# Kernel optimization log

Measured on AMD Instinct MI355X. Metric: run time of the kernel, lower is better.

The kernel has to match this reference:

```python
import jax, jax.numpy as jnp
import numpy as np

DIM = 256
N_STATE = 8
DT_RANK = 16  # ceil(dim/16)
D_CONV = 4
HIDDEN = 128  # dim * rank_ratio
EPS = 1e-6


def rmsnorm(x, w):
    # matches torch: x / (||x||_2 / sqrt(d) + eps) * w
    norm = jnp.sqrt(jnp.sum(x * x, axis=-1, keepdims=True))
    return x / (norm / np.sqrt(x.shape[-1]) + EPS) * w


def dwconv1d(x, w, b, pad_l, pad_r):
    # x: (b, l, c); w: (c, 1, k) depthwise
    out = jax.lax.conv_general_dilated(
        x.transpose(0, 2, 1), w, window_strides=(1,),
        padding=[(pad_l, pad_r)], dimension_numbers=('NCH', 'OIH', 'NCH'),
        feature_group_count=w.shape[0])
    return (out + b[None, :, None]).transpose(0, 2, 1)


def selective_scan(x, delta, A, Bm, Cm, D):
    # x, delta: (b,l,d); A: (d,n); Bm, Cm: (b,l,n); D: (d,)
    dA = jnp.exp(delta[..., None] * A)                     # (b,l,d,n)
    dBx = (delta * x)[..., None] * Bm[:, :, None, :]       # (b,l,d,n)

    def step(h, inp):
        dA_t, dBx_t, C_t = inp
        h = dA_t * h + dBx_t                               # (b,d,n)
        y = jnp.einsum('bdn,bn->bd', h, C_t)
        return h, y

    h0 = jnp.zeros((x.shape[0],) + A.shape, dtype=x.dtype)
    _, ys = jax.lax.scan(step, h0,
                         (dA.transpose(1, 0, 2, 3), dBx.transpose(1, 0, 2, 3),
                          Cm.transpose(1, 0, 2)))
    return ys.transpose(1, 0, 2) + x * D                   # (b,l,d)


def mamba_branch(x, ctx, conv_w, conv_b, xproj_w, dtproj_w, dtproj_b, A_log, D):
    xc = jax.nn.silu(dwconv1d(x, conv_w, conv_b, D_CONV - 1, 0))  # causal conv
    x_dbl = ctx @ xproj_w.T                                  # (b,l,r+2n)
    dt, Bm, Cm = jnp.split(x_dbl, [DT_RANK, DT_RANK + N_STATE], axis=-1)
    delta = jax.nn.softplus(dt @ dtproj_w.T + dtproj_b)
    A = -jnp.exp(A_log)
    return selective_scan(xc, delta, A, Bm, Cm, D)


def setup_inputs() -> dict:
    key = jax.random.key(0)
    ks = jax.random.split(key, 24)
    B, L, D = 4, 64 * 64, DIM
    s = 0.02
    A_log_init = jnp.log(jnp.broadcast_to(jnp.arange(1, N_STATE + 1, dtype=jnp.float32), (D, N_STATE)))
    dt_bias = jnp.full((D,), jnp.log(jnp.expm1(0.01)), dtype=jnp.float32)
    inp = {
        'x0': jax.random.normal(ks[0], (B, L, D), jnp.float32),
        'x1': jax.random.normal(ks[1], (B, L, D), jnp.float32),
        'w_norm0': jnp.ones((D,), jnp.float32),
        'w_norm1': jnp.ones((D,), jnp.float32),
        'in_proj_w': jax.random.normal(ks[2], (2 * D, D), jnp.float32) * s,
        'conv_w_f': jax.random.normal(ks[3], (D, 1, D_CONV), jnp.float32) * 0.3,
        'conv_b_f': jnp.zeros((D,), jnp.float32),
        'xproj_w_f': jax.random.normal(ks[4], (DT_RANK + 2 * N_STATE, D), jnp.float32) * s,
        'dtproj_w_f': jax.random.normal(ks[5], (D, DT_RANK), jnp.float32) * 0.1,
        'dtproj_b_f': dt_bias,
        'A_log_f': A_log_init,
        'D_f': jnp.ones((D,), jnp.float32),
        'conv_w_bw': jax.random.normal(ks[6], (D, 1, D_CONV), jnp.float32) * 0.3,
        'conv_b_bw': jnp.zeros((D,), jnp.float32),
        'xproj_w_bw': jax.random.normal(ks[7], (DT_RANK + 2 * N_STATE, D), jnp.float32) * s,
        'dtproj_w_bw': jax.random.normal(ks[8], (D, DT_RANK), jnp.float32) * 0.1,
        'dtproj_b_bw': dt_bias,
        'A_log_bw': A_log_init,
        'D_bw': jnp.ones((D,), jnp.float32),
        'norm_y_w': jnp.ones((D,), jnp.float32),
        'out_proj_w': jax.random.normal(ks[9], (D, D), jnp.float32) * s,
        'fc1_w': jax.random.normal(ks[10], (HIDDEN, D), jnp.float32) * s,
        'dw_w': jax.random.normal(ks[11], (HIDDEN, 1, 3), jnp.float32) * 0.3,
        'dw_b': jnp.zeros((HIDDEN,), jnp.float32),
        'fc2_w': jax.random.normal(ks[12], (D, HIDDEN), jnp.float32) * s,
    }
    return inp


def reference(x0, x1, w_norm0, w_norm1, in_proj_w, conv_w_f, conv_b_f, xproj_w_f,
              dtproj_w_f, dtproj_b_f, A_log_f, D_f, conv_w_bw, conv_b_bw,
              xproj_w_bw, dtproj_w_bw, dtproj_b_bw, A_log_bw, D_bw, norm_y_w,
              out_proj_w, fc1_w, dw_w, dw_b, fc2_w):
    residual = x0
    h0 = rmsnorm(x0, w_norm0)
    h1 = rmsnorm(x1, w_norm1)
    # cross-Mamba: main stream x0 -> x,z; extra_emb x1 -> dt/B/C
    xz = h0 @ in_proj_w.T
    xin, z = jnp.split(xz, 2, axis=-1)
    y_f = mamba_branch(xin, h1, conv_w_f, conv_b_f, xproj_w_f, dtproj_w_f,
                       dtproj_b_f, A_log_f, D_f)
    y_b = jnp.flip(mamba_branch(jnp.flip(xin, 1), jnp.flip(h1, 1), conv_w_bw,
                                conv_b_bw, xproj_w_bw, dtproj_w_bw, dtproj_b_bw,
                                A_log_bw, D_bw), 1)
    y = (y_f + y_b) * 0.5          # if_devide_out=True (bidirectional)
    y = rmsnorm(y, norm_y_w)       # use_norm=True
    y = y * jax.nn.silu(z)
    x = y @ out_proj_w.T + residual
    # LowRankFeedForward (dropout = identity at eval)
    m = x @ fc1_w.T
    m = jax.nn.silu(dwconv1d(m, dw_w, dw_b, 1, 1))
    m = m @ fc2_w.T
    return x + m
```

## Files before the change

kernel.cpp:

```cpp
#include <hip/hip_runtime.h>
#include <math.h>
#include <cstddef>

#define BB 4
#define LL 4096
#define DD 256
#define NST 8
#define RANK 16
#define HID 128
#define BL (BB*LL)
#define BLD ((size_t)BL*DD)
#define CH 256
#define CLEN 16
#define XZS 512

typedef __bf16 bf16x8 __attribute__((ext_vector_type(8)));
typedef float  f32x4  __attribute__((ext_vector_type(4)));

__device__ __forceinline__ float siluf(float x){ return x / (1.f + __expf(-x)); }
__device__ __forceinline__ float softplus_fast(float x){
  float r = __logf(1.f + __expf(x));
  return x > 15.f ? x : r;
}
__device__ __forceinline__ unsigned short f2bf(float x){
  union { float f; unsigned u; } v; v.f = x;
  unsigned r = v.u + 0x7fffu + ((v.u >> 16) & 1u);
  return (unsigned short)(r >> 16);
}
__device__ __forceinline__ float bf2f(unsigned short u){
  union { unsigned u32; float f; } c; c.u32 = ((unsigned)u) << 16;
  return c.f;
}

__global__ __launch_bounds__(64) void rms_kernel(
    const float* __restrict__ x0, const float* __restrict__ w0, unsigned short* __restrict__ o0b,
    const float* __restrict__ x1, const float* __restrict__ w1, unsigned short* __restrict__ o1b)
{
  const float* x; const float* w; unsigned short* o;
  if (blockIdx.y == 0){ x = x0; w = w0; o = o0b; } else { x = x1; w = w1; o = o1b; }
  size_t tok = blockIdx.x;
  int lane = threadIdx.x;
  float4 v = ((const float4*)(x + tok*DD))[lane];
  float s = v.x*v.x + v.y*v.y + v.z*v.z + v.w*v.w;
  #pragma unroll
  for (int m = 1; m < 64; m <<= 1) s += __shfl_xor(s, m, 64);
  float scale = 1.f / (sqrtf(s) * (1.f/16.f) + 1e-6f);
  float4 wv = ((const float4*)w)[lane];
  ushort4 r;
  r.x = f2bf(v.x*scale*wv.x); r.y = f2bf(v.y*scale*wv.y);
  r.z = f2bf(v.z*scale*wv.z); r.w = f2bf(v.w*scale*wv.w);
  ((ushort4*)(o + tok*DD))[lane] = r;
}

__global__ __launch_bounds__(256) void cvt1_kernel(
    const float* __restrict__ s, unsigned short* __restrict__ d, int n)
{
  int i = blockIdx.x*256 + threadIdx.x;
  if (i < n) d[i] = f2bf(s[i]);
}
__global__ __launch_bounds__(256) void cvt5_kernel(
    const float* __restrict__ s0, const float* __restrict__ s1,
    const float* __restrict__ s2, const float* __restrict__ s3,
    const float* __restrict__ s4, unsigned short* __restrict__ d)
{
  int i = blockIdx.x*256 + threadIdx.x;
  if (i >= 147456) return;
  float v;
  if (i < 8192)        v = s0[i];
  else if (i < 16384)  v = s1[i - 8192];
  else if (i < 81920)  v = s2[i - 16384];
  else if (i < 114688) v = s3[i - 81920];
  else                 v = s4[i - 114688];
  d[i] = f2bf(v);
}

template<int EPI>
__global__ __launch_bounds__(256) void gemm_mfma(
    const unsigned short* __restrict__ A, const unsigned short* __restrict__ Bw,
    float* __restrict__ C, const float* __restrict__ Add,
    unsigned short* __restrict__ Cb, int M, int ldc, int K)
{
  constexpr int BK = 32, PAD = 8;
  __shared__ __align__(16) unsigned short As[64][BK+PAD];
  __shared__ __align__(16) unsigned short Bs[64][BK+PAD];
  int tid  = threadIdx.x;
  int row0 = blockIdx.x * 64;
  int col0 = blockIdx.y * 64;
  int wave = tid >> 6, lane = tid & 63;
  int wm = (wave >> 1) * 32, wn = (wave & 1) * 32;
  int lm = lane & 15, kq = lane >> 4;
  int sr = tid >> 2, sc8 = (tid & 3) * 8;

  f32x4 acc[2][2];
  #pragma unroll
  for (int i = 0; i < 2; i++)
    #pragma unroll
    for (int j = 0; j < 2; j++) acc[i][j] = (f32x4){0.f,0.f,0.f,0.f};

  for (int k0 = 0; k0 < K; k0 += BK){
    *(int4*)&As[sr][sc8] = *(const int4*)&A [(size_t)(row0 + sr)*K + k0 + sc8];
    *(int4*)&Bs[sr][sc8] = *(const int4*)&Bw[(size_t)(col0 + sr)*K + k0 + sc8];
    __syncthreads();
    bf16x8 af[2], bfv[2];
    #pragma unroll
    for (int i = 0; i < 2; i++) af[i]  = *(const bf16x8*)&As[wm + i*16 + lm][kq*8];
    #pragma unroll
    for (int j = 0; j < 2; j++) bfv[j] = *(const bf16x8*)&Bs[wn + j*16 + lm][kq*8];
    #pragma unroll
    for (int i = 0; i < 2; i++)
      #pragma unroll
      for (int j = 0; j < 2; j++)
        acc[i][j] = __builtin_amdgcn_mfma_f32_16x16x32_bf16(af[i], bfv[j], acc[i][j], 0, 0, 0);
    __syncthreads();
  }

  #pragma unroll
  for (int i = 0; i < 2; i++){
    int rbase = row0 + wm + i*16 + kq*4;
    #pragma unroll
    for (int j = 0; j < 2; j++){
      int col = col0 + wn + j*16 + lm;
      #pragma unroll
      for (int r = 0; r < 4; r++){
        size_t idx = (size_t)(rbase + r)*ldc + col;
        float v = acc[i][j][r];
        if constexpr (EPI == 1 || EPI == 2) v += Add[idx];
        if constexpr (EPI != 3) C[idx] = v;
        if constexpr (EPI == 1 || EPI == 3) Cb[idx] = f2bf(v);
      }
    }
  }
}

__global__ __launch_bounds__(256) void front_kernel(
    const unsigned short* __restrict__ xz,
    const float* __restrict__ xd,
    const float* __restrict__ cwf, const float* __restrict__ cbf,
    const float* __restrict__ cwb, const float* __restrict__ cbb,
    const float* __restrict__ dtwf, const float* __restrict__ dtbf,
    const float* __restrict__ dtwb, const float* __restrict__ dtbb,
    const float* __restrict__ Alogf, const float* __restrict__ Alogb,
    const float* __restrict__ Dfp, const float* __restrict__ Dbp,
    unsigned int* __restrict__ xde,
    float* __restrict__ Sp, float* __restrict__ Hout)
{
  int chunk = blockIdx.x, b = blockIdx.y, dir = blockIdx.z;
  int s0 = chunk*CLEN;
  int d  = threadIdx.x;

  __shared__ float sdt[CLEN][16];
  __shared__ float sB [CLEN][8];
  __shared__ float sC [CLEN][8];
  #pragma unroll
  for (int e = threadIdx.x; e < CLEN*32; e += 256){
    int lt = e >> 5, col = e & 31;
    int pos = s0 + lt;
    int row = dir ? (LL-1-pos) : pos;
    float v = xd[((size_t)b*LL + row)*64 + dir*32 + col];
    if (col < 16)      sdt[lt][col]    = v;
    else if (col < 24) sB [lt][col-16] = v;
    else               sC [lt][col-24] = v;
  }
  __syncthreads();

  float4 cw = ((const float4*)(dir ? cwb : cwf))[d];
  float cb  = (dir ? cbb : cbf)[d];
  const float* dtw = (dir ? dtwb : dtwf) + d*RANK;
  float4 w0 = ((const float4*)dtw)[0], w1 = ((const float4*)dtw)[1];
  float4 w2 = ((const float4*)dtw)[2], w3 = ((const float4*)dtw)[3];
  float dtb = (dir ? dtbb : dtbf)[d];
  float Dd  = (dir ? Dbp : Dfp)[d];

  const unsigned short* xp = xz + (size_t)b*LL*XZS + d;
  #define LDX(pos) ((pos) >= 0 ? bf2f(xp[(size_t)(dir ? (LL-1-(pos)) : (pos))*XZS]) : 0.f)

  float xv[CLEN+3];
  xv[0] = LDX(s0-3); xv[1] = LDX(s0-2); xv[2] = LDX(s0-1);
  #pragma unroll
  for (int i = 0; i < CLEN; i++) xv[3+i] = LDX(s0+i);
  #undef LDX

  unsigned packX[CLEN];
  #pragma unroll
  for (int i = 0; i < CLEN; i++){
    float xc = cb;
    xc = fmaf(cw.x, xv[i],   xc); xc = fmaf(cw.y, xv[i+1], xc);
    xc = fmaf(cw.z, xv[i+2], xc); xc = fmaf(cw.w, xv[i+3], xc);
    xc = siluf(xc);
    const float* dt = &sdt[i][0];
    float de = dtb;
    de = fmaf(dt[0],w0.x, fmaf(dt[1],w0.y, fmaf(dt[2],w0.z, fmaf(dt[3],w0.w, de))));
    de = fmaf(dt[4],w1.x, fmaf(dt[5],w1.y, fmaf(dt[6],w1.z, fmaf(dt[7],w1.w, de))));
    de = fmaf(dt[8],w2.x, fmaf(dt[9],w2.y, fmaf(dt[10],w2.z, fmaf(dt[11],w2.w, de))));
    de = fmaf(dt[12],w3.x, fmaf(dt[13],w3.y, fmaf(dt[14],w3.z, fmaf(dt[15],w3.w, de))));
    de = softplus_fast(de);
    packX[i] = (unsigned)f2bf(xc) | ((unsigned)f2bf(de) << 16);
  }

  const float* Alog = dir ? Alogb : Alogf;
  float A[NST];
  bool fast = true;
  #pragma unroll
  for (int n = 0; n < NST; n++){
    A[n] = -__expf(Alog[d*NST + n]);
    fast = fast && (fabsf(A[n] + (float)(n+1)) < 1e-3f);
  }
  float h[NST];
  #pragma unroll
  for (int n = 0; n < NST; n++) h[n] = 0.f;
  float S = 0.f;

  unsigned int* xout = xde + ((size_t)(dir*BB + b)*LL + s0)*DD + d;

  if (fast){
    #pragma unroll
    for (int t = 0; t < CLEN; t++){
      unsigned pk = packX[t];
      float xc = bf2f((unsigned short)(pk & 0xffffu));
      float de = bf2f((unsigned short)(pk >> 16));
      S += de;
      float dux = de * xc;
      const float* Bv = &sB[t][0];
      const float* Cv = &sC[t][0];
      float e1 = __expf(-de);
      float dA = e1;
      float acc = xc * Dd;
      h[0] = fmaf(dA, h[0], dux*Bv[0]); acc = fmaf(h[0], Cv[0], acc); dA *= e1;
      h[1] = fmaf(dA, h[1], dux*Bv[1]); acc = fmaf(h[1], Cv[1], acc); dA *= e1;
      h[2] = fmaf(dA, h[2], dux*Bv[2]); acc = fmaf(h[2], Cv[2], acc); dA *= e1;
      h[3] = fmaf(dA, h[3], dux*Bv[3]); acc = fmaf(h[3], Cv[3], acc); dA *= e1;
      h[4] = fmaf(dA, h[4], dux*Bv[4]); acc = fmaf(h[4], Cv[4], acc); dA *= e1;
      h[5] = fmaf(dA, h[5], dux*Bv[5]); acc = fmaf(h[5], Cv[5], acc); dA *= e1;
      h[6] = fmaf(dA, h[6], dux*Bv[6]); acc = fmaf(h[6], Cv[6], acc); dA *= e1;
      h[7] = fmaf(dA, h[7], dux*Bv[7]); acc = fmaf(h[7], Cv[7], acc);
      xout[(size_t)t*DD] = (pk & 0xffff0000u) | (unsigned)f2bf(acc);
    }
  } else {
    #pragma unroll
    for (int t = 0; t < CLEN; t++){
      unsigned pk = packX[t];
      float xc = bf2f((unsigned short)(pk & 0xffffu));
      float de = bf2f((unsigned short)(pk >> 16));
      S += de;
      float dux = de * xc;
      const float* Bv = &sB[t][0];
      const float* Cv = &sC[t][0];
      float acc = xc * Dd;
      #pragma unroll
      for (int n = 0; n < NST; n++){
        h[n] = fmaf(__expf(de*A[n]), h[n], dux*Bv[n]);
        acc = fmaf(h[n], Cv[n], acc);
      }
      xout[(size_t)t*DD] = (pk & 0xffff0000u) | (unsigned)f2bf(acc);
    }
  }

  size_t ob = ((((size_t)dir*CH + chunk)*BB + b)*DD + d)*NST;
  float4 h0v, h1v;
  h0v.x=h[0]; h0v.y=h[1]; h0v.z=h[2]; h0v.w=h[3];
  h1v.x=h[4]; h1v.y=h[5]; h1v.z=h[6]; h1v.w=h[7];
  *(float4*)&Hout[ob]   = h0v; *(float4*)&Hout[ob+4] = h1v;
  Sp[((size_t)(dir*CH + chunk)*BB + b)*DD + d] = S;
}

__global__ __launch_bounds__(64) void scan_p2(
    const float* __restrict__ Sp, float* H,
    const float* __restrict__ Alogf, const float* __restrict__ Alogb)
{
  const int SEGC = CH/8;
  int blk = blockIdx.x;
  int d   = blk & (DD-1);
  int b   = (blk >> 8) & (BB-1);
  int dir = blk >> 10;
  int t   = threadIdx.x;
  int seg = t >> 3, n = t & 7;
  float A = -__expf((dir ? Alogb : Alogf)[d*NST + n]);

  const size_t sstr = (size_t)BB*DD;
  const size_t hstr = (size_t)BB*DD*NST;
  size_t sb = (size_t)dir*CH*sstr + (size_t)b*DD + d;
  size_t hb = (size_t)dir*CH*hstr + ((size_t)b*DD + d)*NST + n;
  int c0 = seg*SEGC;

  float pv[SEGC], hv[SEGC];
  #pragma unroll
  for (int k = 0; k < SEGC; k++){
    pv[k] = Sp[sb + (size_t)(c0+k)*sstr];
    hv[k] = H [hb + (size_t)(c0+k)*hstr];
  }
  float h = 0.f, Ss = 0.f;
  #pragma unroll
  for (int k = 0; k < SEGC; k++){
    Ss += pv[k];
    pv[k] = __expf(pv[k]*A);
    h = fmaf(pv[k], h, hv[k]);
  }
  float pi = __expf(Ss*A), hi = h;
  #pragma unroll
  for (int off = 8; off < 64; off <<= 1){
    float hprev = __shfl_up(hi, off, 64);
    float pprev = __shfl_up(pi, off, 64);
    if (t >= off){ hi = fmaf(pi, hprev, hi); pi *= pprev; }
  }
  float hin = __shfl_up(hi, 8, 64);
  h = (seg == 0) ? 0.f : hin;
  #pragma unroll
  for (int k = 0; k < SEGC; k++){
    size_t idx = hb + (size_t)(c0+k)*hstr;
    H[idx] = h;
    h = fmaf(pv[k], h, hv[k]);
  }
}

__global__ __launch_bounds__(256) void scan_corr(
    const unsigned int* __restrict__ xde,
    const float* __restrict__ xd,
    const float* __restrict__ Alogf, const float* __restrict__ Alogb,
    const float* __restrict__ Hin,
    unsigned short* __restrict__ yf, unsigned short* __restrict__ yb)
{
  int chunk = blockIdx.x, b = blockIdx.y, dir = blockIdx.z;
  int d = threadIdx.x;
  int base = chunk*CLEN;

  __shared__ float sC[CLEN][8];
  if (threadIdx.x < CLEN*8){
    int lt = threadIdx.x >> 3, col = threadIdx.x & 7;
    int pos = base + lt;
    int row = dir ? (LL-1-pos) : pos;
    sC[lt][col] = xd[((size_t)b*LL + row)*64 + dir*32 + 24 + col];
  }
  __syncthreads();

  const float* Alog = dir ? Alogb : Alogf;
  float A[NST];
  bool fast = true;
  #pragma unroll
  for (int n = 0; n < NST; n++){
    A[n] = -__expf(Alog[d*NST + n]);
    fast = fast && (fabsf(A[n] + (float)(n+1)) < 1e-3f);
  }
  float hn[NST];
  {
    size_t ib = ((((size_t)dir*CH + chunk)*BB + b)*DD + d)*NST;
    float4 a0 = *(const float4*)&Hin[ib];
    float4 a1 = *(const float4*)&Hin[ib+4];
    hn[0]=a0.x; hn[1]=a0.y; hn[2]=a0.z; hn[3]=a0.w;
    hn[4]=a1.x; hn[5]=a1.y; hn[6]=a1.z; hn[7]=a1.w;
  }

  const unsigned int* xdep = xde + ((size_t)(dir*BB + b)*LL + base)*DD + d;
  unsigned short* yp = (dir ? yb : yf) + ((size_t)b*LL + base)*DD + d;

  unsigned int pk[CLEN];
  #pragma unroll
  for (int t = 0; t < CLEN; t++) pk[t] = xdep[(size_t)t*DD];

  float S = 0.f;
  if (fast){
    #pragma unroll
    for (int t = 0; t < CLEN; t++){
      float y0 = bf2f((unsigned short)(pk[t] & 0xffffu));
      float de = bf2f((unsigned short)(pk[t] >> 16));
      S += de;
      float E = __expf(-S);
      float q = E;
      float corr = q * (hn[0]*sC[t][0]);
      q *= E; corr = fmaf(q, hn[1]*sC[t][1], corr);
      q *= E; corr = fmaf(q, hn[2]*sC[t][2], corr);
      q *= E; corr = fmaf(q, hn[3]*sC[t][3], corr);
      q *= E; corr = fmaf(q, hn[4]*sC[t][4], corr);
      q *= E; corr = fmaf(q, hn[5]*sC[t][5], corr);
      q *= E; corr = fmaf(q, hn[6]*sC[t][6], corr);
      q *= E; corr = fmaf(q, hn[7]*sC[t][7], corr);
      yp[(size_t)t*DD] = f2bf(y0 + corr);
    }
  } else {
    #pragma unroll
    for (int t = 0; t < CLEN; t++){
      float y0 = bf2f((unsigned short)(pk[t] & 0xffffu));
      float de = bf2f((unsigned short)(pk[t] >> 16));
      S += de;
      float corr = 0.f;
      #pragma unroll
      for (int n = 0; n < NST; n++)
        corr = fmaf(__expf(S*A[n]), hn[n]*sC[t][n], corr);
      yp[(size_t)t*DD] = f2bf(y0 + corr);
    }
  }
}

__global__ __launch_bounds__(64) void combine_kernel(
    const unsigned short* __restrict__ yf, const unsigned short* __restrict__ yb,
    const unsigned short* __restrict__ xz, const float* __restrict__ wn,
    unsigned short* __restrict__ outb)
{
  size_t tok = blockIdx.x;
  int b = (int)(tok / LL), t = (int)(tok % LL);
  int lane = threadIdx.x;
  ushort4 au = ((const ushort4*)(yf + tok*DD))[lane];
  ushort4 cu = ((const ushort4*)(yb + ((size_t)b*LL + (LL-1-t))*DD))[lane];
  float4 v;
  v.x=(bf2f(au.x)+bf2f(cu.x))*0.5f; v.y=(bf2f(au.y)+bf2f(cu.y))*0.5f;
  v.z=(bf2f(au.z)+bf2f(cu.z))*0.5f; v.w=(bf2f(au.w)+bf2f(cu.w))*0.5f;
  float s = v.x*v.x + v.y*v.y + v.z*v.z + v.w*v.w;
  #pragma unroll
  for (int m = 1; m < 64; m <<= 1) s += __shfl_xor(s, m, 64);
  float scale = 1.f / (sqrtf(s)*(1.f/16.f) + 1e-6f);
  float4 wv = ((const float4*)wn)[lane];
  ushort4 zv = *(const ushort4*)&xz[tok*XZS + 256 + lane*4];
  ushort4 r;
  r.x = f2bf(v.x*scale*wv.x*siluf(bf2f(zv.x)));
  r.y = f2bf(v.y*scale*wv.y*siluf(bf2f(zv.y)));
  r.z = f2bf(v.z*scale*wv.z*siluf(bf2f(zv.z)));
  r.w = f2bf(v.w*scale*wv.w*siluf(bf2f(zv.w)));
  ((ushort4*)(outb + tok*DD))[lane] = r;
}

__global__ __launch_bounds__(256) void dwconv3_kernel(
    const float* __restrict__ m, const float* __restrict__ w,
    const float* __restrict__ bi, unsigned short* __restrict__ o)
{
  size_t gid = (size_t)blockIdx.x*256 + threadIdx.x;
  int c = (int)(gid % HID);
  int tok = (int)(gid / HID);
  int b = tok / LL, t = tok % LL;
  float acc = bi[c];
  #pragma unroll
  for (int k = 0; k < 3; k++){
    int tt = t - 1 + k;
    if (tt >= 0 && tt < LL)
      acc = fmaf(w[c*3 + k], m[((size_t)b*LL + tt)*HID + c], acc);
  }
  o[gid] = f2bf(siluf(acc));
}

extern "C" void kernel_launch(void* const* d_in, const int* in_sizes, int n_in,
                              void* d_out, int out_size, void* d_ws, size_t ws_size,
                              hipStream_t stream)
{
  const float* x0        = (const float*)d_in[0];
  const float* x1        = (const float*)d_in[1];
  const float* w_norm0   = (const float*)d_in[2];
  const float* w_norm1   = (const float*)d_in[3];
  const float* in_proj_w = (const float*)d_in[4];
  const float* conv_w_f  = (const float*)d_in[5];
  const float* conv_b_f  = (const float*)d_in[6];
  const float* xproj_w_f = (const float*)d_in[7];
  const float* dtproj_w_f= (const float*)d_in[8];
  const float* dtproj_b_f= (const float*)d_in[9];
  const float* A_log_f   = (const float*)d_in[10];
  const float* D_f       = (const float*)d_in[11];
  const float* conv_w_bw = (const float*)d_in[12];
  const float* conv_b_bw = (const float*)d_in[13];
  const float* xproj_w_bw= (const float*)d_in[14];
  const float* dtproj_w_bw=(const float*)d_in[15];
  const float* dtproj_b_bw=(const float*)d_in[16];
  const float* A_log_bw  = (const float*)d_in[17];
  const float* D_bw      = (const float*)d_in[18];
  const float* norm_y_w  = (const float*)d_in[19];
  const float* out_proj_w= (const float*)d_in[20];
  const float* fc1_w     = (const float*)d_in[21];
  const float* dw_w      = (const float*)d_in[22];
  const float* dw_b      = (const float*)d_in[23];
  const float* fc2_w     = (const float*)d_in[24];
  float* out = (float*)d_out;
  float* ws  = (float*)d_ws;

  float* r0 = ws + 0*BLD;
  float* r1 = ws + 1*BLD;
  float* r2 = ws + 2*BLD;
  float* r3 = ws + 3*BLD;
  float* r4 = ws + 4*BLD;
  float* r5 = ws + 5*BLD;
  float* r6 = ws + 6*BLD;
  float* r7 = ws + 7*BLD;

  unsigned short* h0b   = (unsigned short*)r0;
  unsigned short* h1b   = (unsigned short*)r1;
  unsigned short* xz_b  = (unsigned short*)r2;
  float*          xd    = r3;
  unsigned int*   xde   = (unsigned int*)r4;
  unsigned short* wbuf1 = (unsigned short*)r6;
  unsigned short* yfb   = (unsigned short*)r0;
  unsigned short* ybb   = (unsigned short*)r1;
  float* Hout = r6;
  float* Hin  = Hout;
  const size_t SPLANE = (size_t)2*CH*BB*DD;
  float* Sp   = r7 + (BLD - SPLANE);
  unsigned short* ycomb_b = (unsigned short*)r3;
  unsigned short* wbuf2   = (unsigned short*)r7;
  unsigned short* wb_xp   = wbuf2;
  unsigned short* wb_out  = wbuf2 + 16384;
  unsigned short* wb_fc1  = wbuf2 + 81920;
  unsigned short* wb_fc2  = wbuf2 + 114688;
  unsigned short* xb      = wbuf2 + 147456;
  float*          m1      = r4;
  unsigned short* m2b     = (unsigned short*)r5;

  cvt1_kernel<<<dim3(512), 256, 0, stream>>>(in_proj_w, wbuf1, 131072);
  cvt5_kernel<<<dim3(576), 256, 0, stream>>>(
      xproj_w_f, xproj_w_bw, out_proj_w, fc1_w, fc2_w, wbuf2);

  rms_kernel<<<dim3(BL,2), 64, 0, stream>>>(x0, w_norm0, h0b, x1, w_norm1, h1b);

  gemm_mfma<3><<<dim3(BL/64, 8), 256, 0, stream>>>(
      h0b, wbuf1, nullptr, nullptr, xz_b, BL, XZS, 256);

  gemm_mfma<0><<<dim3(BL/64, 1), 256, 0, stream>>>(
      h1b, wb_xp, xd, nullptr, nullptr, BL, 64, 256);

  front_kernel<<<dim3(CH, BB, 2), 256, 0, stream>>>(
      xz_b, xd, conv_w_f, conv_b_f, conv_w_bw, conv_b_bw,
      dtproj_w_f, dtproj_b_f, dtproj_w_bw, dtproj_b_bw,
      A_log_f, A_log_bw, D_f, D_bw, xde, Sp, Hout);

  scan_p2<<<dim3(2*BB*DD), 64, 0, stream>>>(Sp, Hout, A_log_f, A_log_bw);

  scan_corr<<<dim3(CH, BB, 2), 256, 0, stream>>>(
      xde, xd, A_log_f, A_log_bw, Hin, yfb, ybb);

  combine_kernel<<<dim3(BL), 64, 0, stream>>>(yfb, ybb, xz_b, norm_y_w, ycomb_b);

  gemm_mfma<1><<<dim3(BL/64, 4), 256, 0, stream>>>(
      ycomb_b, wb_out, out, x0, xb, BL, 256, 256);

  gemm_mfma<0><<<dim3(BL/64, 2), 256, 0, stream>>>(
      xb, wb_fc1, m1, nullptr, nullptr, BL, 128, 256);

  dwconv3_kernel<<<dim3((BL*HID)/256), 256, 0, stream>>>(m1, dw_w, dw_b, m2b);

  gemm_mfma<2><<<dim3(BL/64, 4), 256, 0, stream>>>(
      m2b, wb_fc2, out, out, nullptr, BL, 256, 128);
}
```

Baseline: 262.3 us.

## Fuse scan correction with combine/rmsnorm/gate; widen GEMM K tile; interleave front compute

Replaces the separate scan_corr and combine kernels with a single back_kernel. Each block handles a forward chunk and its mirrored backward chunk, averages the two directions in registers, does the RMS norm with a cross-wave shared-memory reduction, and applies the SiLU(z) gate. This removes the bf16 y_f/y_b round trip through global memory and one launch. It also doubles the GEMM K tile to 64, which halves the number of barriers per tile, and moves the front conv/delta computation into the scan loop instead of first packing it into an array. The costs are more shared memory and registers per block, fewer blocks in the back stage, and column-strided per-token output writes.

```diff
diff --git a/kernel.cpp b/kernel.cpp
--- a/kernel.cpp
+++ b/kernel.cpp
@@ -80,7 +80,7 @@
     float* __restrict__ C, const float* __restrict__ Add,
     unsigned short* __restrict__ Cb, int M, int ldc, int K)
 {
-  constexpr int BK = 32, PAD = 8;
+  constexpr int BK = 64, PAD = 8;
   __shared__ __align__(16) unsigned short As[64][BK+PAD];
   __shared__ __align__(16) unsigned short Bs[64][BK+PAD];
   int tid  = threadIdx.x;
@@ -89,7 +89,7 @@
   int wave = tid >> 6, lane = tid & 63;
   int wm = (wave >> 1) * 32, wn = (wave & 1) * 32;
   int lm = lane & 15, kq = lane >> 4;
-  int sr = tid >> 2, sc8 = (tid & 3) * 8;
+  int sr = tid >> 2, sc16 = (tid & 3) * 16;
 
   f32x4 acc[2][2];
   #pragma unroll
@@ -98,19 +98,26 @@
     for (int j = 0; j < 2; j++) acc[i][j] = (f32x4){0.f,0.f,0.f,0.f};
 
   for (int k0 = 0; k0 < K; k0 += BK){
-    *(int4*)&As[sr][sc8] = *(const int4*)&A [(size_t)(row0 + sr)*K + k0 + sc8];
-    *(int4*)&Bs[sr][sc8] = *(const int4*)&Bw[(size_t)(col0 + sr)*K + k0 + sc8];
+    const unsigned short* ap = &A [(size_t)(row0 + sr)*K + k0 + sc16];
+    const unsigned short* bp = &Bw[(size_t)(col0 + sr)*K + k0 + sc16];
+    *(int4*)&As[sr][sc16]   = *(const int4*)ap;
+    *(int4*)&As[sr][sc16+8] = *(const int4*)(ap + 8);
+    *(int4*)&Bs[sr][sc16]   = *(const int4*)bp;
+    *(int4*)&Bs[sr][sc16+8] = *(const int4*)(bp + 8);
     __syncthreads();
-    bf16x8 af[2], bfv[2];
-    #pragma unroll
-    for (int i = 0; i < 2; i++) af[i]  = *(const bf16x8*)&As[wm + i*16 + lm][kq*8];
-    #pragma unroll
-    for (int j = 0; j < 2; j++) bfv[j] = *(const bf16x8*)&Bs[wn + j*16 + lm][kq*8];
-    #pragma unroll
-    for (int i = 0; i < 2; i++)
-      #pragma unroll
-      for (int j = 0; j < 2; j++)
-        acc[i][j] = __builtin_amdgcn_mfma_f32_16x16x32_bf16(af[i], bfv[j], acc[i][j], 0, 0, 0);
+    #pragma unroll
+    for (int ks = 0; ks < 2; ks++){
+      bf16x8 af[2], bfv[2];
+      #pragma unroll
+      for (int i = 0; i < 2; i++) af[i]  = *(const bf16x8*)&As[wm + i*16 + lm][ks*32 + kq*8];
+      #pragma unroll
+      for (int j = 0; j < 2; j++) bfv[j] = *(const bf16x8*)&Bs[wn + j*16 + lm][ks*32 + kq*8];
+      #pragma unroll
+      for (int i = 0; i < 2; i++)
+        #pragma unroll
+        for (int j = 0; j < 2; j++)
+          acc[i][j] = __builtin_amdgcn_mfma_f32_16x16x32_bf16(af[i], bfv[j], acc[i][j], 0, 0, 0);
+    }
     __syncthreads();
   }
 
@@ -171,32 +178,6 @@
   float dtb = (dir ? dtbb : dtbf)[d];
   float Dd  = (dir ? Dbp : Dfp)[d];
 
-  const unsigned short* xp = xz + (size_t)b*LL*XZS + d;
-  #define LDX(pos) ((pos) >= 0 ? bf2f(xp[(size_t)(dir ? (LL-1-(pos)) : (pos))*XZS]) : 0.f)
-
-  float xv[CLEN+3];
-  xv[0] = LDX(s0-3); xv[1] = LDX(s0-2); xv[2] = LDX(s0-1);
-  #pragma unroll
-  for (int i = 0; i < CLEN; i++) xv[3+i] = LDX(s0+i);
-  #undef LDX
-
-  unsigned packX[CLEN];
-  #pragma unroll
-  for (int i = 0; i < CLEN; i++){
-    float xc = cb;
-    xc = fmaf(cw.x, xv[i],   xc); xc = fmaf(cw.y, xv[i+1], xc);
-    xc = fmaf(cw.z, xv[i+2], xc); xc = fmaf(cw.w, xv[i+3], xc);
-    xc = siluf(xc);
-    const float* dt = &sdt[i][0];
-    float de = dtb;
-    de = fmaf(dt[0],w0.x, fmaf(dt[1],w0.y, fmaf(dt[2],w0.z, fmaf(dt[3],w0.w, de))));
-    de = fmaf(dt[4],w1.x, fmaf(dt[5],w1.y, fmaf(dt[6],w1.z, fmaf(dt[7],w1.w, de))));
-    de = fmaf(dt[8],w2.x, fmaf(dt[9],w2.y, fmaf(dt[10],w2.z, fmaf(dt[11],w2.w, de))));
-    de = fmaf(dt[12],w3.x, fmaf(dt[13],w3.y, fmaf(dt[14],w3.z, fmaf(dt[15],w3.w, de))));
-    de = softplus_fast(de);
-    packX[i] = (unsigned)f2bf(xc) | ((unsigned)f2bf(de) << 16);
-  }
-
   const float* Alog = dir ? Alogb : Alogf;
   float A[NST];
   bool fast = true;
@@ -205,26 +186,47 @@
     A[n] = -__expf(Alog[d*NST + n]);
     fast = fast && (fabsf(A[n] + (float)(n+1)) < 1e-3f);
   }
+
+  const unsigned short* xp = xz + (size_t)b*LL*XZS + d;
+  #define LDX(pos) ((pos) >= 0 ? bf2f(xp[(size_t)(dir ? (LL-1-(pos)) : (pos))*XZS]) : 0.f)
+  float xv[CLEN+3];
+  xv[0] = LDX(s0-3); xv[1] = LDX(s0-2); xv[2] = LDX(s0-1);
+  #pragma unroll
+  for (int i = 0; i < CLEN; i++) xv[3+i] = LDX(s0+i);
+  #undef LDX
+
   float h[NST];
   #pragma unroll
   for (int n = 0; n < NST; n++) h[n] = 0.f;
   float S = 0.f;
-
   unsigned int* xout = xde + ((size_t)(dir*BB + b)*LL + s0)*DD + d;
 
+  #define FRONT_STEP(i, xcb, deb, dbits)                                           \
+    float xc = cb;                                                                 \
+    xc = fmaf(cw.x, xv[i],   xc); xc = fmaf(cw.y, xv[i+1], xc);                    \
+    xc = fmaf(cw.z, xv[i+2], xc); xc = fmaf(cw.w, xv[i+3], xc);                    \
+    xc = siluf(xc);                                                                \
+    const float* dt = &sdt[i][0];                                                  \
+    float de = dtb;                                                                \
+    de = fmaf(dt[0],w0.x, fmaf(dt[1],w0.y, fmaf(dt[2],w0.z, fmaf(dt[3],w0.w, de))));\
+    de = fmaf(dt[4],w1.x, fmaf(dt[5],w1.y, fmaf(dt[6],w1.z, fmaf(dt[7],w1.w, de))));\
+    de = fmaf(dt[8],w2.x, fmaf(dt[9],w2.y, fmaf(dt[10],w2.z, fmaf(dt[11],w2.w, de))));\
+    de = fmaf(dt[12],w3.x, fmaf(dt[13],w3.y, fmaf(dt[14],w3.z, fmaf(dt[15],w3.w, de))));\
+    de = softplus_fast(de);                                                        \
+    unsigned short dbits = f2bf(de);                                               \
+    float xcb = bf2f(f2bf(xc)), deb = bf2f(dbits);
+
   if (fast){
     #pragma unroll
-    for (int t = 0; t < CLEN; t++){
-      unsigned pk = packX[t];
-      float xc = bf2f((unsigned short)(pk & 0xffffu));
-      float de = bf2f((unsigned short)(pk >> 16));
-      S += de;
-      float dux = de * xc;
-      const float* Bv = &sB[t][0];
-      const float* Cv = &sC[t][0];
-      float e1 = __expf(-de);
+    for (int i = 0; i < CLEN; i++){
+      FRONT_STEP(i, xcb, deb, dbits)
+      S += deb;
+      float dux = deb * xcb;
+      const float* Bv = &sB[i][0];
+      const float* Cv = &sC[i][0];
+      float e1 = __expf(-deb);
       float dA = e1;
-      float acc = xc * Dd;
+      float acc = xcb * Dd;
       h[0] = fmaf(dA, h[0], dux*Bv[0]); acc = fmaf(h[0], Cv[0], acc); dA *= e1;
       h[1] = fmaf(dA, h[1], dux*Bv[1]); acc = fmaf(h[1], Cv[1], acc); dA *= e1;
       h[2] = fmaf(dA, h[2], dux*Bv[2]); acc = fmaf(h[2], Cv[2], acc); dA *= e1;
@@ -233,27 +235,26 @@
       h[5] = fmaf(dA, h[5], dux*Bv[5]); acc = fmaf(h[5], Cv[5], acc); dA *= e1;
       h[6] = fmaf(dA, h[6], dux*Bv[6]); acc = fmaf(h[6], Cv[6], acc); dA *= e1;
       h[7] = fmaf(dA, h[7], dux*Bv[7]); acc = fmaf(h[7], Cv[7], acc);
-      xout[(size_t)t*DD] = (pk & 0xffff0000u) | (unsigned)f2bf(acc);
+      xout[(size_t)i*DD] = ((unsigned)dbits << 16) | (unsigned)f2bf(acc);
     }
   } else {
     #pragma unroll
-    for (int t = 0; t < CLEN; t++){
-      unsigned pk = packX[t];
-      float xc = bf2f((unsigned short)(pk & 0xffffu));
-      float de = bf2f((unsigned short)(pk >> 16));
-      S += de;
-      float dux = de * xc;
-      const float* Bv = &sB[t][0];
-      const float* Cv = &sC[t][0];
-      float acc = xc * Dd;
+    for (int i = 0; i < CLEN; i++){
+      FRONT_STEP(i, xcb, deb, dbits)
+      S += deb;
+      float dux = deb * xcb;
+      const float* Bv = &sB[i][0];
+      const float* Cv = &sC[i][0];
+      float acc = xcb * Dd;
       #pragma unroll
       for (int n = 0; n < NST; n++){
-        h[n] = fmaf(__expf(de*A[n]), h[n], dux*Bv[n]);
+        h[n] = fmaf(__expf(deb*A[n]), h[n], dux*Bv[n]);
         acc = fmaf(h[n], Cv[n], acc);
       }
-      xout[(size_t)t*DD] = (pk & 0xffff0000u) | (unsigned)f2bf(acc);
+      xout[(size_t)i*DD] = ((unsigned)dbits << 16) | (unsigned)f2bf(acc);
     }
   }
+  #undef FRONT_STEP
 
   size_t ob = ((((size_t)dir*CH + chunk)*BB + b)*DD + d)*NST;
   float4 h0v, h1v;
@@ -312,109 +313,160 @@
   }
 }
 
-__global__ __launch_bounds__(256) void scan_corr(
+__global__ __launch_bounds__(256) void back_kernel(
     const unsigned int* __restrict__ xde,
     const float* __restrict__ xd,
     const float* __restrict__ Alogf, const float* __restrict__ Alogb,
     const float* __restrict__ Hin,
-    unsigned short* __restrict__ yf, unsigned short* __restrict__ yb)
-{
-  int chunk = blockIdx.x, b = blockIdx.y, dir = blockIdx.z;
-  int d = threadIdx.x;
-  int base = chunk*CLEN;
-
-  __shared__ float sC[CLEN][8];
-  if (threadIdx.x < CLEN*8){
-    int lt = threadIdx.x >> 3, col = threadIdx.x & 7;
-    int pos = base + lt;
-    int row = dir ? (LL-1-pos) : pos;
-    sC[lt][col] = xd[((size_t)b*LL + row)*64 + dir*32 + 24 + col];
+    const unsigned short* __restrict__ xz,
+    const float* __restrict__ wn,
+    unsigned short* __restrict__ outb)
+{
+  int c  = blockIdx.x, b = blockIdx.y;
+  int cbk = CH-1-c;
+  int d  = threadIdx.x;
+  int T0 = c*CLEN;
+  int Pb = cbk*CLEN;
+
+  __shared__ float sCf[CLEN][8], sCb[CLEN][8];
+  __shared__ float red[CLEN][4];
+  __shared__ float sscale[CLEN];
+  {
+    int k  = threadIdx.x & 7;
+    int lt = (threadIdx.x >> 3) & 15;
+    if (threadIdx.x < 128)
+      sCf[lt][k] = xd[((size_t)b*LL + T0 + lt)*64 + 24 + k];
+    else
+      sCb[lt][k] = xd[((size_t)b*LL + (T0 + 15 - lt))*64 + 56 + k];
   }
   __syncthreads();
 
-  const float* Alog = dir ? Alogb : Alogf;
-  float A[NST];
+  float Af[NST], Ab[NST];
   bool fast = true;
   #pragma unroll
   for (int n = 0; n < NST; n++){
-    A[n] = -__expf(Alog[d*NST + n]);
-    fast = fast && (fabsf(A[n] + (float)(n+1)) < 1e-3f);
-  }
-  float hn[NST];
+    Af[n] = -__expf(Alogf[d*NST + n]);
+    Ab[n] = -__expf(Alogb[d*NST + n]);
+    fast = fast && (fabsf(Af[n] + (float)(n+1)) < 1e-3f)
+                && (fabsf(Ab[n] + (float)(n+1)) < 1e-3f);
+  }
+
+  float vf[CLEN];
+
   {
-    size_t ib = ((((size_t)dir*CH + chunk)*BB + b)*DD + d)*NST;
+    float hn[NST];
+    size_t ib = (((size_t)c*BB + b)*DD + d)*NST;
     float4 a0 = *(const float4*)&Hin[ib];
     float4 a1 = *(const float4*)&Hin[ib+4];
     hn[0]=a0.x; hn[1]=a0.y; hn[2]=a0.z; hn[3]=a0.w;
     hn[4]=a1.x; hn[5]=a1.y; hn[6]=a1.z; hn[7]=a1.w;
-  }
-
-  const unsigned int* xdep = xde + ((size_t)(dir*BB + b)*LL + base)*DD + d;
-  unsigned short* yp = (dir ? yb : yf) + ((size_t)b*LL + base)*DD + d;
-
-  unsigned int pk[CLEN];
-  #pragma unroll
-  for (int t = 0; t < CLEN; t++) pk[t] = xdep[(size_t)t*DD];
-
-  float S = 0.f;
-  if (fast){
-    #pragma unroll
-    for (int t = 0; t < CLEN; t++){
-      float y0 = bf2f((unsigned short)(pk[t] & 0xffffu));
-      float de = bf2f((unsigned short)(pk[t] >> 16));
-      S += de;
-      float E = __expf(-S);
-      float q = E;
-      float corr = q * (hn[0]*sC[t][0]);
-      q *= E; corr = fmaf(q, hn[1]*sC[t][1], corr);
-      q *= E; corr = fmaf(q, hn[2]*sC[t][2], corr);
-      q *= E; corr = fmaf(q, hn[3]*sC[t][3], corr);
-      q *= E; corr = fmaf(q, hn[4]*sC[t][4], corr);
-      q *= E; corr = fmaf(q, hn[5]*sC[t][5], corr);
-      q *= E; corr = fmaf(q, hn[6]*sC[t][6], corr);
-      q *= E; corr = fmaf(q, hn[7]*sC[t][7], corr);
-      yp[(size_t)t*DD] = f2bf(y0 + corr);
+    const unsigned int* p = xde + ((size_t)b*LL + T0)*DD + d;
+    unsigned int pk[CLEN];
+    #pragma unroll
+    for (int t = 0; t < CLEN; t++) pk[t] = p[(size_t)t*DD];
+    float S = 0.f;
+    if (fast){
+      #pragma unroll
+      for (int t = 0; t < CLEN; t++){
+        float y0 = bf2f((unsigned short)(pk[t] & 0xffffu));
+        float de = bf2f((unsigned short)(pk[t] >> 16));
+        S += de;
+        float E = __expf(-S);
+        float q = E;
+        float corr = q * (hn[0]*sCf[t][0]);
+        q *= E; corr = fmaf(q, hn[1]*sCf[t][1], corr);
+        q *= E; corr = fmaf(q, hn[2]*sCf[t][2], corr);
+        q *= E; corr = fmaf(q, hn[3]*sCf[t][3], corr);
+        q *= E; corr = fmaf(q, hn[4]*sCf[t][4], corr);
+        q *= E; corr = fmaf(q, hn[5]*sCf[t][5], corr);
+        q *= E; corr = fmaf(q, hn[6]*sCf[t][6], corr);
+        q *= E; corr = fmaf(q, hn[7]*sCf[t][7], corr);
+        vf[t] = y0 + corr;
+      }
+    } else {
+      #pragma unroll
+      for (int t = 0; t < CLEN; t++){
+        float y0 = bf2f((unsigned short)(pk[t] & 0xffffu));
+        float de = bf2f((unsigned short)(pk[t] >> 16));
+        S += de;
+        float corr = 0.f;
+        #pragma unroll
+        for (int n = 0; n < NST; n++)
+          corr = fmaf(__expf(S*Af[n]), hn[n]*sCf[t][n], corr);
+        vf[t] = y0 + corr;
+      }
     }
-  } else {
-    #pragma unroll
-    for (int t = 0; t < CLEN; t++){
-      float y0 = bf2f((unsigned short)(pk[t] & 0xffffu));
-      float de = bf2f((unsigned short)(pk[t] >> 16));
-      S += de;
-      float corr = 0.f;
-      #pragma unroll
-      for (int n = 0; n < NST; n++)
-        corr = fmaf(__expf(S*A[n]), hn[n]*sC[t][n], corr);
-      yp[(size_t)t*DD] = f2bf(y0 + corr);
+  }
+
+  {
+    float hn[NST];
+    size_t ib = ((((size_t)CH + cbk)*BB + b)*DD + d)*NST;
+    float4 a0 = *(const float4*)&Hin[ib];
+    float4 a1 = *(const float4*)&Hin[ib+4];
+    hn[0]=a0.x; hn[1]=a0.y; hn[2]=a0.z; hn[3]=a0.w;
+    hn[4]=a1.x; hn[5]=a1.y; hn[6]=a1.z; hn[7]=a1.w;
+    const unsigned int* p = xde + ((size_t)(BB + b)*LL + Pb)*DD + d;
+    unsigned int pk[CLEN];
+    #pragma unroll
+    for (int t = 0; t < CLEN; t++) pk[t] = p[(size_t)t*DD];
+    float S = 0.f;
+    if (fast){
+      #pragma unroll
+      for (int t = 0; t < CLEN; t++){
+        float y0 = bf2f((unsigned short)(pk[t] & 0xffffu));
+        float de = bf2f((unsigned short)(pk[t] >> 16));
+        S += de;
+        float E = __expf(-S);
+        float q = E;
+        float corr = q * (hn[0]*sCb[t][0]);
+        q *= E; corr = fmaf(q, hn[1]*sCb[t][1], corr);
+        q *= E; corr = fmaf(q, hn[2]*sCb[t][2], corr);
+        q *= E; corr = fmaf(q, hn[3]*sCb[t][3], corr);
+        q *= E; corr = fmaf(q, hn[4]*sCb[t][4], corr);
+        q *= E; corr = fmaf(q, hn[5]*sCb[t][5], corr);
+        q *= E; corr = fmaf(q, hn[6]*sCb[t][6], corr);
+        q *= E; corr = fmaf(q, hn[7]*sCb[t][7], corr);
+        int j = 15 - t;
+        vf[j] = 0.5f*(vf[j] + y0 + corr);
+      }
+    } else {
+      #pragma unroll
+      for (int t = 0; t < CLEN; t++){
+        float y0 = bf2f((unsigned short)(pk[t] & 0xffffu));
+        float de = bf2f((unsigned short)(pk[t] >> 16));
+        S += de;
+        float corr = 0.f;
+        #pragma unroll
+        for (int n = 0; n < NST; n++)
+          corr = fmaf(__expf(S*Ab[n]), hn[n]*sCb[t][n], corr);
+        int j = 15 - t;
+        vf[j] = 0.5f*(vf[j] + y0 + corr);
+      }
     }
   }
-}
-
-__global__ __launch_bounds__(64) void combine_kernel(
-    const unsigned short* __restrict__ yf, const unsigned short* __restrict__ yb,
-    const unsigned short* __restrict__ xz, const float* __restrict__ wn,
-    unsigned short* __restrict__ outb)
-{
-  size_t tok = blockIdx.x;
-  int b = (int)(tok / LL), t = (int)(tok % LL);
-  int lane = threadIdx.x;
-  ushort4 au = ((const ushort4*)(yf + tok*DD))[lane];
-  ushort4 cu = ((const ushort4*)(yb + ((size_t)b*LL + (LL-1-t))*DD))[lane];
-  float4 v;
-  v.x=(bf2f(au.x)+bf2f(cu.x))*0.5f; v.y=(bf2f(au.y)+bf2f(cu.y))*0.5f;
-  v.z=(bf2f(au.z)+bf2f(cu.z))*0.5f; v.w=(bf2f(au.w)+bf2f(cu.w))*0.5f;
-  float s = v.x*v.x + v.y*v.y + v.z*v.z + v.w*v.w;
-  #pragma unroll
-  for (int m = 1; m < 64; m <<= 1) s += __shfl_xor(s, m, 64);
-  float scale = 1.f / (sqrtf(s)*(1.f/16.f) + 1e-6f);
-  float4 wv = ((const float4*)wn)[lane];
-  ushort4 zv = *(const ushort4*)&xz[tok*XZS + 256 + lane*4];
-  ushort4 r;
-  r.x = f2bf(v.x*scale*wv.x*siluf(bf2f(zv.x)));
-  r.y = f2bf(v.y*scale*wv.y*siluf(bf2f(zv.y)));
-  r.z = f2bf(v.z*scale*wv.z*siluf(bf2f(zv.z)));
-  r.w = f2bf(v.w*scale*wv.w*siluf(bf2f(zv.w)));
-  ((ushort4*)(outb + tok*DD))[lane] = r;
+
+  int wave = d >> 6, lane = d & 63;
+  #pragma unroll
+  for (int j = 0; j < CLEN; j++){
+    float s = vf[j]*vf[j];
+    #pragma unroll
+    for (int m = 1; m < 64; m <<= 1) s += __shfl_xor(s, m, 64);
+    if (lane == 0) red[j][wave] = s;
+  }
+  __syncthreads();
+  if (d < CLEN){
+    float s = red[d][0] + red[d][1] + red[d][2] + red[d][3];
+    sscale[d] = 1.f / (sqrtf(s)*(1.f/16.f) + 1e-6f);
+  }
+  __syncthreads();
+
+  float wd = wn[d];
+  #pragma unroll
+  for (int j = 0; j < CLEN; j++){
+    size_t tok = (size_t)b*LL + T0 + j;
+    float z = bf2f(xz[tok*XZS + 256 + d]);
+    outb[tok*DD + d] = f2bf(vf[j]*sscale[j]*wd*siluf(z));
+  }
 }
 
 __global__ __launch_bounds__(256) void dwconv3_kernel(
@@ -482,13 +534,11 @@
   float*          xd    = r3;
   unsigned int*   xde   = (unsigned int*)r4;
   unsigned short* wbuf1 = (unsigned short*)r6;
-  unsigned short* yfb   = (unsigned short*)r0;
-  unsigned short* ybb   = (unsigned short*)r1;
   float* Hout = r6;
   float* Hin  = Hout;
   const size_t SPLANE = (size_t)2*CH*BB*DD;
   float* Sp   = r7 + (BLD - SPLANE);
-  unsigned short* ycomb_b = (unsigned short*)r3;
+  unsigned short* ycomb_b = (unsigned short*)r0;
   unsigned short* wbuf2   = (unsigned short*)r7;
   unsigned short* wb_xp   = wbuf2;
   unsigned short* wb_out  = wbuf2 + 16384;
@@ -517,10 +567,8 @@
 
   scan_p2<<<dim3(2*BB*DD), 64, 0, stream>>>(Sp, Hout, A_log_f, A_log_bw);
 
-  scan_corr<<<dim3(CH, BB, 2), 256, 0, stream>>>(
-      xde, xd, A_log_f, A_log_bw, Hin, yfb, ybb);
-
-  combine_kernel<<<dim3(BL), 64, 0, stream>>>(yfb, ybb, xz_b, norm_y_w, ycomb_b);
+  back_kernel<<<dim3(CH, BB), 256, 0, stream>>>(
+      xde, xd, A_log_f, A_log_bw, Hin, xz_b, norm_y_w, ycomb_b);
 
   gemm_mfma<1><<<dim3(BL/64, 4), 256, 0, stream>>>(
       ycomb_b, wb_out, out, x0, xb, BL, 256, 256);
```

After: 263.6 us. No clear change (+0.5%).
